# Kernel optimization log

Measured on AMD Instinct MI355X. Metric: run time of the kernel, lower is better.

The kernel has to match this reference:

```python
import jax, jax.numpy as jnp
import numpy as np

N = 64
NUM_INPUTS = 6
NUM_OUTPUTS = 2
T_STEPS = 1024
BATCH = 1024
DT = 1.0
TAU = 10.0
ALPHA = DT / TAU
SIGMA_REC = 0.03
SIGMA_INP = 0.03
SLOPE = 1.0  # activation_slope for relu


def setup_inputs() -> dict:
    key = jax.random.key(0)
    k_u, k_rn, k_in, k_wi, k_wr, k_wo = jax.random.split(key, 6)
    u = jax.random.normal(k_u, (NUM_INPUTS, T_STEPS, BATCH), dtype=jnp.float32)
    rec_noise = jax.random.normal(k_rn, (N, T_STEPS, BATCH), dtype=jnp.float32)
    inp_noise = jax.random.normal(k_in, (NUM_INPUTS, T_STEPS, BATCH), dtype=jnp.float32)
    # learned params (masks are all-ones, already folded in)
    W_inp = jax.random.normal(k_wi, (N, NUM_INPUTS), dtype=jnp.float32) * 0.3
    W_rec = jax.random.normal(k_wr, (N, N), dtype=jnp.float32) * (0.9 / np.sqrt(N))
    W_out = jax.random.normal(k_wo, (NUM_OUTPUTS, N), dtype=jnp.float32) * 0.3
    return {"u": u, "rec_noise": rec_noise, "inp_noise": inp_noise,
            "W_inp": W_inp, "W_rec": W_rec, "W_out": W_out}


def _forward(u, rec_noise, inp_noise, W_inp, W_rec, W_out):
    # scale standard-normal noise exactly as torch: sqrt(2/alpha * sigma^2) * randn
    rn = jnp.sqrt(2.0 / ALPHA) * SIGMA_REC * rec_noise   # (N, T, B)
    inn = jnp.sqrt(2.0 / ALPHA) * SIGMA_INP * inp_noise  # (num_inputs, T, B)
    # move to (T, B, feat) for scan
    u_t = jnp.transpose(u, (1, 2, 0))     # (T, B, num_inputs)
    rn_t = jnp.transpose(rn, (1, 2, 0))   # (T, B, N)
    inn_t = jnp.transpose(inn, (1, 2, 0)) # (T, B, num_inputs)
    x0 = jnp.zeros((BATCH, N), dtype=u.dtype)  # self.x = zeros(N), broadcast over batch

    def step(x, inp):
        u_i, rn_i, in_i = inp
        pre = x @ W_rec.T + (u_i + in_i) @ W_inp.T
        act = jnp.maximum(0.0, SLOPE * pre)
        x_new = (1.0 - ALPHA) * x + ALPHA * (act + rn_i)
        return x_new, x_new

    # the torch loop runs T_steps-1 iterations using inputs at steps 0..T-2
    _, xs = jax.lax.scan(step, x0, (u_t[:-1], rn_t[:-1], inn_t[:-1]))
    states_tbn = jnp.concatenate([x0[None], xs], axis=0)  # (T, B, N)
    outputs_tbo = states_tbn @ W_out.T                    # (T, B, num_outputs)
    states = jnp.transpose(states_tbn, (2, 0, 1))   # (N, T, B)
    outputs = jnp.transpose(outputs_tbo, (2, 0, 1)) # (num_outputs, T, B)
    return states, outputs


def reference(u, rec_noise, inp_noise, W_inp, W_rec, W_out):
    return _forward(u, rec_noise, inp_noise, W_inp, W_rec, W_out)
```

## Files before the change

kernel.cpp:

```cpp
#include <hip/hip_runtime.h>

#define NN 64
#define NI 6
#define TT 1024
#define BB 1024
#define TB (TT * BB)
#define NSCALE 0.13416407864998738f
#define ARNSCALE 0.013416407864998739f
#define SW 68
#define SX 72

#define BARRIER() do {                                                        \
    __builtin_amdgcn_sched_barrier(0);                                        \
    asm volatile("s_waitcnt lgkmcnt(0)\n\ts_barrier" ::: "memory");           \
    __builtin_amdgcn_sched_barrier(0);                                        \
} while (0)

__global__ __launch_bounds__(256, 1) void latent_rnn(
    const float* __restrict__ u,
    const float* __restrict__ rn,
    const float* __restrict__ inn,
    const float* __restrict__ Winp,
    const float* __restrict__ Wrec,
    float* __restrict__ states)
{
    const int hw  = blockIdx.x;
    const int lb  = (hw & 7) * 32 + (hw >> 3);
    const int b0  = lb * 4;
    const int tid = threadIdx.x;
    const int n   = tid >> 2;
    const int b   = tid & 3;
    const int gb  = b0 + b;

    __shared__ __align__(16) float wlds[NN * SW];
    __shared__ __align__(16) float xb[2][4][SX];

    {
        const float4* src = (const float4*)Wrec;
#pragma unroll
        for (int j = 0; j < 4; ++j) {
            const int f4   = tid * 4 + j;
            const int flat = f4 * 4;
            *(float4*)&wlds[(flat >> 6) * SW + (flat & 63)] = src[f4];
        }
    }

    float wi[NI];
#pragma unroll
    for (int i = 0; i < NI; ++i) wi[i] = Winp[n * NI + i];

    xb[0][b][n] = 0.0f;
    xb[1][b][n] = 0.0f;

    const bool stage = (tid < NI * 4);
    const float* usrc = u   + n * TB + gb;
    const float* isrc = inn + n * TB + gb;
    float su0 = 0.f, su1 = 0.f, si0 = 0.f, si1 = 0.f;
    if (stage) {
        xb[0][b][64 + n] = fmaf(NSCALE, isrc[0], usrc[0]);
        su1 = usrc[1 * BB]; si1 = isrc[1 * BB];
        su0 = usrc[2 * BB]; si0 = isrc[2 * BB];
    }

    states[n * TB + gb] = 0.0f;

    __syncthreads();

    float wreg[NN];
    {
        const float4* wrow = (const float4*)&wlds[n * SW];
#pragma unroll
        for (int k4 = 0; k4 < 16; ++k4) {
            const float4 wv = wrow[k4];
            wreg[4*k4+0] = wv.x; wreg[4*k4+1] = wv.y;
            wreg[4*k4+2] = wv.z; wreg[4*k4+3] = wv.w;
        }
    }

    const float* rsrc = rn + n * TB + gb;
    float* sdst = states + n * TB + gb;

    float rnb[4];
#pragma unroll
    for (int d = 0; d < 4; ++d) rnb[d] = rsrc[d * BB];

    float xreg = 0.0f;

#define STEP(tcur, slot, CC, SS)                                              \
  {                                                                           \
    const float rcur = rnb[slot];                                             \
    { int tp = (tcur) + 4; if (tp > TT - 1) tp = TT - 1;                      \
      rnb[slot] = rsrc[tp * BB]; }                                            \
    const float4* xrow = (const float4*)&xb[CC][b][0];                        \
    float a0 = 0.f, a1 = 0.f, a2 = 0.f, a3 = 0.f;                             \
    _Pragma("unroll")                                                         \
    for (int k4 = 0; k4 < 16; ++k4) {                                         \
        const float4 xv = xrow[k4];                                           \
        a0 = fmaf(xv.x, wreg[4*k4+0], a0);                                    \
        a1 = fmaf(xv.y, wreg[4*k4+1], a1);                                    \
        a2 = fmaf(xv.z, wreg[4*k4+2], a2);                                    \
        a3 = fmaf(xv.w, wreg[4*k4+3], a3);                                    \
    }                                                                         \
    const float4 iv0 = xrow[16];                                              \
    const float4 iv1 = xrow[17];                                              \
    a0 = fmaf(iv0.x, wi[0], a0); a1 = fmaf(iv0.y, wi[1], a1);                 \
    a2 = fmaf(iv0.z, wi[2], a2); a3 = fmaf(iv0.w, wi[3], a3);                 \
    a0 = fmaf(iv1.x, wi[4], a0); a1 = fmaf(iv1.y, wi[5], a1);                 \
    const float pre = (a0 + a1) + (a2 + a3);                                  \
    const float xn  = fmaf(0.9f, xreg,                                        \
                           fmaf(0.1f, fmaxf(pre, 0.f), ARNSCALE * rcur));     \
    xreg = xn;                                                                \
    sdst[((tcur) + 1) * BB] = xn;                                             \
    xb[(CC) ^ 1][b][n] = xn;                                                  \
    if (stage) {                                                              \
        xb[(CC) ^ 1][b][64 + n] =                                             \
            fmaf(NSCALE, (SS) ? si1 : si0, (SS) ? su1 : su0);                 \
        int tp3 = (tcur) + 3; if (tp3 > TT - 1) tp3 = TT - 1;                 \
        if (SS) { su1 = usrc[tp3 * BB]; si1 = isrc[tp3 * BB]; }               \
        else    { su0 = usrc[tp3 * BB]; si0 = isrc[tp3 * BB]; }               \
    }                                                                         \
    BARRIER();                                                                \
  }

#pragma unroll 1
    for (int t = 0; t < 1020; t += 4) {
        STEP(t + 0, 0, 0, 1);
        STEP(t + 1, 1, 1, 0);
        STEP(t + 2, 2, 0, 1);
        STEP(t + 3, 3, 1, 0);
    }
    STEP(1020, 0, 0, 1);
    STEP(1021, 1, 1, 0);
    STEP(1022, 2, 0, 1);
#undef STEP
}

__global__ __launch_bounds__(256) void out_proj(
    const float* __restrict__ states,
    const float* __restrict__ Wout,
    float* __restrict__ outputs)
{
    const int g4 = (blockIdx.x * 256 + threadIdx.x) * 4;
    float4 a0 = {0.f, 0.f, 0.f, 0.f};
    float4 a1 = {0.f, 0.f, 0.f, 0.f};
#pragma unroll
    for (int k = 0; k < NN; ++k) {
        const float4 s = *reinterpret_cast<const float4*>(states + k * TB + g4);
        const float w0 = Wout[k];
        const float w1 = Wout[NN + k];
        a0.x = fmaf(s.x, w0, a0.x); a0.y = fmaf(s.y, w0, a0.y);
        a0.z = fmaf(s.z, w0, a0.z); a0.w = fmaf(s.w, w0, a0.w);
        a1.x = fmaf(s.x, w1, a1.x); a1.y = fmaf(s.y, w1, a1.y);
        a1.z = fmaf(s.z, w1, a1.z); a1.w = fmaf(s.w, w1, a1.w);
    }
    *reinterpret_cast<float4*>(outputs + g4)      = a0;
    *reinterpret_cast<float4*>(outputs + TB + g4) = a1;
}

extern "C" void kernel_launch(void* const* d_in, const int* in_sizes, int n_in,
                              void* d_out, int out_size, void* d_ws, size_t ws_size,
                              hipStream_t stream) {
    const float* u    = (const float*)d_in[0];
    const float* rn   = (const float*)d_in[1];
    const float* inn  = (const float*)d_in[2];
    const float* Winp = (const float*)d_in[3];
    const float* Wrec = (const float*)d_in[4];
    const float* Wout = (const float*)d_in[5];

    float* states  = (float*)d_out;
    float* outputs = (float*)d_out + (size_t)NN * TT * BB;

    latent_rnn<<<256, 256, 0, stream>>>(u, rn, inn, Winp, Wrec, states);
    out_proj<<<1024, 256, 0, stream>>>(states, Wout, outputs);
}
```

Measured before the change: 706.3 us.

## Map one wave per batch element and broadcast state via readlane

Each wavefront now owns one batch column, with lane l holding neuron l's state. The recurrent matvec pulls the other neurons' values with readlane broadcasts instead of reading the state vector from LDS. Noise and input are staged into transposed LDS buffers so the per-neuron loads stay coalesced, and the state store is deferred one step and read back from LDS. This drops the 64-wide LDS read per step from the dependent chain, at the cost of 64 readlane operations per step that go through scalar registers.

```diff
diff --git a/kernel.cpp b/kernel.cpp
--- a/kernel.cpp
+++ b/kernel.cpp
@@ -7,14 +7,16 @@
 #define TB (TT * BB)
 #define NSCALE 0.13416407864998738f
 #define ARNSCALE 0.013416407864998739f
-#define SW 68
-#define SX 72
 
 #define BARRIER() do {                                                        \
     __builtin_amdgcn_sched_barrier(0);                                        \
     asm volatile("s_waitcnt lgkmcnt(0)\n\ts_barrier" ::: "memory");           \
     __builtin_amdgcn_sched_barrier(0);                                        \
 } while (0)
+
+__device__ __forceinline__ float rdlane(float v, int l) {
+    return __int_as_float(__builtin_amdgcn_readlane(__float_as_int(v), l));
+}
 
 __global__ __launch_bounds__(256, 1) void latent_rnn(
     const float* __restrict__ u,
@@ -28,81 +30,63 @@
     const int lb  = (hw & 7) * 32 + (hw >> 3);
     const int b0  = lb * 4;
     const int tid = threadIdx.x;
+    const int l   = tid & 63;
+    const int w   = tid >> 6;
     const int n   = tid >> 2;
-    const int b   = tid & 3;
-    const int gb  = b0 + b;
+    const int bs  = tid & 3;
 
-    __shared__ __align__(16) float wlds[NN * SW];
-    __shared__ __align__(16) float xb[2][4][SX];
+    __shared__ float rnT[2][4][NN];
+    __shared__ float iT[2][4][8];
+    __shared__ float xT[2][4][NN];
 
-    {
-        const float4* src = (const float4*)Wrec;
+    float wreg[NN];
 #pragma unroll
-        for (int j = 0; j < 4; ++j) {
-            const int f4   = tid * 4 + j;
-            const int flat = f4 * 4;
-            *(float4*)&wlds[(flat >> 6) * SW + (flat & 63)] = src[f4];
-        }
+    for (int k = 0; k < NN; k += 4) {
+        const float4 w4 = *reinterpret_cast<const float4*>(Wrec + l * NN + k);
+        wreg[k] = w4.x; wreg[k + 1] = w4.y; wreg[k + 2] = w4.z; wreg[k + 3] = w4.w;
     }
-
     float wi[NI];
 #pragma unroll
-    for (int i = 0; i < NI; ++i) wi[i] = Winp[n * NI + i];
+    for (int i = 0; i < NI; ++i) wi[i] = Winp[l * NI + i];
 
-    xb[0][b][n] = 0.0f;
-    xb[1][b][n] = 0.0f;
+    const float* rsrc = rn + n * TB + b0 + bs;
+    float*       sdst = states + n * TB + b0 + bs;
+    const bool  ist  = (tid < NI * 4);
+    const int   ii   = tid >> 2;
+    const int   ib   = tid & 3;
+    const float* usrc = u   + ii * TB + b0 + ib;
+    const float* isrc = inn + ii * TB + b0 + ib;
 
-    const bool stage = (tid < NI * 4);
-    const float* usrc = u   + n * TB + gb;
-    const float* isrc = inn + n * TB + gb;
-    float su0 = 0.f, su1 = 0.f, si0 = 0.f, si1 = 0.f;
-    if (stage) {
-        xb[0][b][64 + n] = fmaf(NSCALE, isrc[0], usrc[0]);
-        su1 = usrc[1 * BB]; si1 = isrc[1 * BB];
-        su0 = usrc[2 * BB]; si0 = isrc[2 * BB];
+    rnT[0][bs][n] = rsrc[0];
+    if (ist) iT[0][ib][ii] = fmaf(NSCALE, isrc[0], usrc[0]);
+    xT[0][w][l] = 0.0f;
+
+    float rnPF[4], uPF[4], iPF[4];
+#pragma unroll
+    for (int d = 0; d < 4; ++d) {
+        rnPF[d] = rsrc[(d + 1) * BB];
+        if (ist) { uPF[d] = usrc[(d + 1) * BB]; iPF[d] = isrc[(d + 1) * BB]; }
     }
-
-    states[n * TB + gb] = 0.0f;
-
     __syncthreads();
-
-    float wreg[NN];
-    {
-        const float4* wrow = (const float4*)&wlds[n * SW];
-#pragma unroll
-        for (int k4 = 0; k4 < 16; ++k4) {
-            const float4 wv = wrow[k4];
-            wreg[4*k4+0] = wv.x; wreg[4*k4+1] = wv.y;
-            wreg[4*k4+2] = wv.z; wreg[4*k4+3] = wv.w;
-        }
-    }
-
-    const float* rsrc = rn + n * TB + gb;
-    float* sdst = states + n * TB + gb;
-
-    float rnb[4];
-#pragma unroll
-    for (int d = 0; d < 4; ++d) rnb[d] = rsrc[d * BB];
 
     float xreg = 0.0f;
 
-#define STEP(tcur, slot, CC, SS)                                              \
+#define STEP(tcur, slot, CC)                                                  \
   {                                                                           \
-    const float rcur = rnb[slot];                                             \
-    { int tp = (tcur) + 4; if (tp > TT - 1) tp = TT - 1;                      \
-      rnb[slot] = rsrc[tp * BB]; }                                            \
-    const float4* xrow = (const float4*)&xb[CC][b][0];                        \
+                \
+    sdst[(tcur) * BB] = xT[CC][bs][n];                                        \
+                                                       \
+    const float rcur = rnT[CC][w][l];                                         \
+    const float4 iv0 = *reinterpret_cast<const float4*>(&iT[CC][w][0]);       \
+    const float2 iv1 = *reinterpret_cast<const float2*>(&iT[CC][w][4]);       \
     float a0 = 0.f, a1 = 0.f, a2 = 0.f, a3 = 0.f;                             \
     _Pragma("unroll")                                                         \
-    for (int k4 = 0; k4 < 16; ++k4) {                                         \
-        const float4 xv = xrow[k4];                                           \
-        a0 = fmaf(xv.x, wreg[4*k4+0], a0);                                    \
-        a1 = fmaf(xv.y, wreg[4*k4+1], a1);                                    \
-        a2 = fmaf(xv.z, wreg[4*k4+2], a2);                                    \
-        a3 = fmaf(xv.w, wreg[4*k4+3], a3);                                    \
+    for (int k = 0; k < NN; k += 4) {                                         \
+        a0 = fmaf(rdlane(xreg, k + 0), wreg[k + 0], a0);                      \
+        a1 = fmaf(rdlane(xreg, k + 1), wreg[k + 1], a1);                      \
+        a2 = fmaf(rdlane(xreg, k + 2), wreg[k + 2], a2);                      \
+        a3 = fmaf(rdlane(xreg, k + 3), wreg[k + 3], a3);                      \
     }                                                                         \
-    const float4 iv0 = xrow[16];                                              \
-    const float4 iv1 = xrow[17];                                              \
     a0 = fmaf(iv0.x, wi[0], a0); a1 = fmaf(iv0.y, wi[1], a1);                 \
     a2 = fmaf(iv0.z, wi[2], a2); a3 = fmaf(iv0.w, wi[3], a3);                 \
     a0 = fmaf(iv1.x, wi[4], a0); a1 = fmaf(iv1.y, wi[5], a1);                 \
@@ -110,29 +94,30 @@
     const float xn  = fmaf(0.9f, xreg,                                        \
                            fmaf(0.1f, fmaxf(pre, 0.f), ARNSCALE * rcur));     \
     xreg = xn;                                                                \
-    sdst[((tcur) + 1) * BB] = xn;                                             \
-    xb[(CC) ^ 1][b][n] = xn;                                                  \
-    if (stage) {                                                              \
-        xb[(CC) ^ 1][b][64 + n] =                                             \
-            fmaf(NSCALE, (SS) ? si1 : si0, (SS) ? su1 : su0);                 \
-        int tp3 = (tcur) + 3; if (tp3 > TT - 1) tp3 = TT - 1;                 \
-        if (SS) { su1 = usrc[tp3 * BB]; si1 = isrc[tp3 * BB]; }               \
-        else    { su0 = usrc[tp3 * BB]; si0 = isrc[tp3 * BB]; }               \
-    }                                                                         \
+                                               \
+    xT[(CC) ^ 1][w][l] = xn;                                                  \
+    rnT[(CC) ^ 1][bs][n] = rnPF[slot];                                        \
+    if (ist) iT[(CC) ^ 1][ib][ii] = fmaf(NSCALE, iPF[slot], uPF[slot]);       \
+                                  \
+    { int tp = (tcur) + 5; if (tp > TT - 2) tp = TT - 2;                      \
+      rnPF[slot] = rsrc[tp * BB];                                             \
+      if (ist) { uPF[slot] = usrc[tp * BB]; iPF[slot] = isrc[tp * BB]; } }    \
     BARRIER();                                                                \
   }
 
 #pragma unroll 1
     for (int t = 0; t < 1020; t += 4) {
-        STEP(t + 0, 0, 0, 1);
-        STEP(t + 1, 1, 1, 0);
-        STEP(t + 2, 2, 0, 1);
-        STEP(t + 3, 3, 1, 0);
+        STEP(t + 0, 0, 0);
+        STEP(t + 1, 1, 1);
+        STEP(t + 2, 2, 0);
+        STEP(t + 3, 3, 1);
     }
-    STEP(1020, 0, 0, 1);
-    STEP(1021, 1, 1, 0);
-    STEP(1022, 2, 0, 1);
+    STEP(1020, 0, 0);
+    STEP(1021, 1, 1);
+    STEP(1022, 2, 0);
 #undef STEP
+
+    sdst[(TT - 1) * BB] = xT[1][bs][n];
 }
 
 __global__ __launch_bounds__(256) void out_proj(
```

Measured after the change: 799.3 us. +13.2%, slower.
